# Optimization experiments

Measured on AMD Instinct MI355X. Metric: run time of the kernel, lower is better.

## Reference

```python
import jax, jax.numpy as jnp
import numpy as np
import math

B, T, C, H = 4, 2048, 1024, 16
D = C // H
NEG = -1.0e9

def setup_inputs() -> dict:
    key = jax.random.key(0)
    k_x, k_wa, k_wp = jax.random.split(key, 3)
    x = jax.random.normal(k_x, (B, T, C), dtype=jnp.float32)
    # causal additive-mask input, shape [B, T, T] as the forward branch expects
    mask = jnp.broadcast_to(jnp.tril(jnp.ones((T, T), dtype=jnp.float32)), (B, T, T))
    W_attn = jax.random.normal(k_wa, (C, 3 * C), dtype=jnp.float32) * (1.0 / math.sqrt(C))
    b_attn = jnp.zeros((3 * C,), dtype=jnp.float32)
    W_proj = jax.random.normal(k_wp, (C, C), dtype=jnp.float32) * (1.0 / math.sqrt(C))
    b_proj = jnp.zeros((C,), dtype=jnp.float32)
    return {"x": x, "mask": mask, "W_attn": W_attn, "b_attn": b_attn,
            "W_proj": W_proj, "b_proj": b_proj}

def reference(x, mask, W_attn, b_attn, W_proj, b_proj):
    # fused QKV projection: [B,T,3C]
    qkv = x @ W_attn + b_attn
    q, k, v = jnp.split(qkv, 3, axis=-1)
    q = q.reshape(B, T, H, D)
    k = k.reshape(B, T, H, D)
    v = v.reshape(B, T, H, D)
    # scores [B,H,T,T]
    att = jnp.einsum('bqhd,bkhd->bhqk', q, k) * (1.0 / math.sqrt(D))
    # additive custom mask: att += -1e9 * (1 - mask), broadcast over heads
    att = att + NEG * (1.0 - mask)[:, None, :, :]
    att = jax.nn.softmax(att, axis=-1)  # dropout p=0 -> identity
    y = jnp.einsum('bhqk,bkhd->bqhd', att, v).reshape(B, T, C)
    return y @ W_proj + b_proj
```

## Files before the change

kernel.cpp:

```cpp
#include <hip/hip_runtime.h>
#include <hip/hip_bf16.h>

#define Bq 4
#define Tq 2048
#define Cq 1024
#define Hq 16
#define Dq 64
#define Mq (Bq*Tq)
#define N3q (3*Cq)

typedef __attribute__((ext_vector_type(8))) short   short8;
typedef __attribute__((ext_vector_type(4))) float   f32x4;
typedef __attribute__((ext_vector_type(4))) unsigned int u32x4;
typedef __attribute__((ext_vector_type(4))) unsigned short ushort4v;
typedef unsigned short u16;
typedef unsigned int u32;

__device__ __forceinline__ void gld_lds16(const u16* g, u16* l) {
  __builtin_amdgcn_global_load_lds(
      (const __attribute__((address_space(1))) unsigned int*)g,
      (__attribute__((address_space(3))) unsigned int*)l, 16, 0, 0);
}

__device__ __forceinline__ u16 f2bf(float f) {
  return __builtin_bit_cast(u16, __float2bfloat16(f));
}
__device__ __forceinline__ u16 f2bf_fast(float f) {
  u32 u = __builtin_bit_cast(u32, f);
  return (u16)((u + 0x8000u) >> 16);
}
__device__ __forceinline__ float fexp2(float x) {
  return __builtin_amdgcn_exp2f(x);
}

__device__ __forceinline__ f32x4 mfma16(short8 a, short8 b, f32x4 c) {
  return __builtin_amdgcn_mfma_f32_16x16x32_bf16(a, b, c, 0, 0, 0);
}

__global__ void cvt_bf16(const float* __restrict__ in, u16* __restrict__ out, int n) {
  int i = (blockIdx.x * 256 + threadIdx.x) * 4;
  if (i < n) {
    float4 v = *(const float4*)(in + i);
    ushort4v o;
    o.x = f2bf_fast(v.x); o.y = f2bf_fast(v.y);
    o.z = f2bf_fast(v.z); o.w = f2bf_fast(v.w);
    *(ushort4v*)(out + i) = o;
  }
}

__global__ void transpose_cvt(const float* __restrict__ in, u16* __restrict__ out,
                              int R, int C) {
  __shared__ float tile[32][33];
  int j0 = blockIdx.x * 32;
  int i0 = blockIdx.y * 32;
  int c = threadIdx.x & 31, r0 = threadIdx.x >> 5;
#pragma unroll
  for (int rr = 0; rr < 32; rr += 8)
    tile[r0 + rr][c] = in[(size_t)(i0 + r0 + rr) * C + j0 + c];
  __syncthreads();
#pragma unroll
  for (int rr = 0; rr < 32; rr += 8) {
    int j = r0 + rr;
    out[(size_t)(j0 + j) * R + i0 + c] = f2bf_fast(tile[c][j]);
  }
}

template<int OUT_MODE>
__global__ __launch_bounds__(256, 2) void gemm_bt(
    const u16* __restrict__ A, const u16* __restrict__ Bt,
    const float* __restrict__ bias, void* __restrict__ Dp,
    int M, int N, int K)
{
  __shared__ __align__(16) u16 lA[2][128 * 64];
  __shared__ __align__(16) u16 lB[2][128 * 64];
  const int t = threadIdx.x;
  const int l = t & 63, w = t >> 6;
  const int bn = blockIdx.x, bm = blockIdx.y;
  const int wr = (w >> 1) * 64, wc = (w & 1) * 64;

  const int srow = t >> 3;
  const int scol = 8 * ((t & 7) ^ (srow & 7));
  const u16* ga = A  + (size_t)(bm * 128 + srow) * K + scol;
  const u16* gb = Bt + (size_t)(bn * 128 + srow) * K + scol;

  f32x4 acc[4][4] = {};

#define STAGE_BT(buf, k0_) {                                              \
    _Pragma("unroll")                                                     \
    for (int c = 0; c < 4; ++c) {                                         \
      gld_lds16(ga + (size_t)(32 * c) * K + (k0_), &lA[buf][c * 2048 + w * 512]); \
      gld_lds16(gb + (size_t)(32 * c) * K + (k0_), &lB[buf][c * 2048 + w * 512]); \
    } }

  STAGE_BT(0, 0);
  asm volatile("s_waitcnt vmcnt(0)" ::: "memory");
  __syncthreads();

  int c2 = 0;
  for (int k0 = 0; k0 < K; k0 += 64) {
    const bool more = (k0 + 64 < K);
    if (more) STAGE_BT(c2 ^ 1, k0 + 64);

    short8 af[4][2], bf[4][2];
#pragma unroll
    for (int m = 0; m < 4; ++m)
#pragma unroll
      for (int kk = 0; kk < 2; ++kk) {
        int ar = wr + m * 16 + (l & 15);
        int slot = (kk * 4 + (l >> 4)) ^ (l & 7);
        af[m][kk] = *(const short8*)&lA[c2][ar * 64 + slot * 8];
        int br = wc + m * 16 + (l & 15);
        bf[m][kk] = *(const short8*)&lB[c2][br * 64 + slot * 8];
      }
    __builtin_amdgcn_s_setprio(1);
#pragma unroll
    for (int kk = 0; kk < 2; ++kk)
#pragma unroll
      for (int m = 0; m < 4; ++m)
#pragma unroll
        for (int n = 0; n < 4; ++n)
          acc[m][n] = mfma16(af[m][kk], bf[n][kk], acc[m][n]);
    __builtin_amdgcn_s_setprio(0);

    if (more) {
      asm volatile("s_waitcnt vmcnt(0)" ::: "memory");
      __syncthreads();
      c2 ^= 1;
    }
  }
#undef STAGE_BT

  float bv[4];
#pragma unroll
  for (int n = 0; n < 4; ++n) bv[n] = bias[bn * 128 + wc + n * 16 + (l & 15)];

  if (OUT_MODE == 2) {
    const int col0 = bn * 128 + wc;
    const int p  = col0 >> 10;
    const int hh = (col0 >> 6) & 15;
    u16* qb = (u16*)Dp;
#pragma unroll
    for (int m = 0; m < 4; ++m)
#pragma unroll
      for (int r = 0; r < 4; ++r) {
        int row = bm * 128 + wr + m * 16 + (l >> 4) * 4 + r;
        int bb = row >> 11, tt = row & 2047;
        u16* dst = qb + (((size_t)(p * 64 + bb * 16 + hh) * 2048 + tt) * 64) + (l & 15);
#pragma unroll
        for (int n = 0; n < 4; ++n)
          dst[n * 16] = f2bf_fast(acc[m][n][r] + bv[n]);
      }
  } else {
#pragma unroll
    for (int m = 0; m < 4; ++m)
#pragma unroll
      for (int r = 0; r < 4; ++r) {
        int row = bm * 128 + wr + m * 16 + (l >> 4) * 4 + r;
        size_t base = (size_t)row * N + bn * 128 + wc + (l & 15);
#pragma unroll
        for (int n = 0; n < 4; ++n)
          ((float*)Dp)[base + n * 16] = acc[m][n][r] + bv[n];
      }
  }
}

__global__ __launch_bounds__(1024, 4) void flash_attn(
    const u16* __restrict__ qkvh, u16* __restrict__ Y)
{
  __shared__ __align__(16) u16 Kl[2][64 * 64];
  __shared__ __align__(16) u16 Vt[2][64 * 64];

  const int t = threadIdx.x, l = t & 63, w = t >> 6;
  const int wg  = w & 3;
  const int g   = l >> 4;
  const int id   = blockIdx.x + 4 * blockIdx.y;
  const int xcd  = id & 7;
  const int rest = id >> 3;
  const int x    = rest & 3;
  const int gg   = rest >> 2;
  const int bh   = xcd + 8 * gg;
  const int b = bh >> 4, h = bh & 15;
  const int grp = w >> 2;
  const int qA = 4 * x + grp, qB = 31 - qA;
  const int jmaxb = 31 - 4 * x;

  const size_t hbase = (size_t)(b * Hq + h) * (size_t)(Tq * Dq);
  const u16* Qh = qkvh + hbase;
  const u16* Kh = qkvh + (size_t)64  * (Tq * Dq) + hbase;
  const u16* Vh = qkvh + (size_t)128 * (Tq * Dq) + hbase;

  short8 qfA[2], qfB[2];
  {
    const u16* qp = Qh + (size_t)(qA * 64 + wg * 16 + (l & 15)) * 64;
    qfA[0] = *(const short8*)(qp + (g * 8));
    qfA[1] = *(const short8*)(qp + 32 + (g * 8));
    const u16* qp2 = Qh + (size_t)(qB * 64 + wg * 16 + (l & 15)) * 64;
    qfB[0] = *(const short8*)(qp2 + (g * 8));
    qfB[1] = *(const short8*)(qp2 + 32 + (g * 8));
  }

  float mA = -1e30f, lsA = 0.f, mB = -1e30f, lsB = 0.f;
  f32x4 oA[4] = {}, oB[4] = {};

  const int ksrow = t >> 3;
  const int kscol = 8 * ((t & 7) ^ (ksrow & 7));
  const int vkey = t & 63;
  const int vdj  = w - 8;

  const int srcA = ((g << 1) & 3) * 16 + (l & 15);
  const int srcB = (((g << 1) + 1) & 3) * 16 + (l & 15);
  const bool sel = (g >> 1) != 0;

  if (w < 8) {
    gld_lds16(Kh + (size_t)ksrow * 64 + kscol, &Kl[0][w * 512]);
  } else {
    short8 vr = *(const short8*)(Vh + (size_t)vkey * 64 + vdj * 8);
    asm volatile("s_waitcnt vmcnt(0)" ::: "memory");
#pragma unroll
    for (int i = 0; i < 8; ++i)
      Vt[0][(vdj * 8 + i) * 64 + (((vkey >> 3) ^ i) * 8) + (vkey & 7)] = (u16)vr[i];
  }
  __syncthreads();

  int cur = 0;
  for (int j = 0; j <= jmaxb; ++j) {
    short8 vrn;
    if (j < jmaxb) {
      const size_t krow1 = (size_t)(j + 1) * 64;
      if (w < 8)
        gld_lds16(Kh + (krow1 + ksrow) * 64 + kscol, &Kl[cur ^ 1][w * 512]);
      else
        vrn = *(const short8*)(Vh + (krow1 + vkey) * 64 + vdj * 8);
    }

#pragma unroll
    for (int strip = 0; strip < 2; ++strip) {
      const int qb = strip ? qB : qA;
      if (j > qb) continue;
      const short8* qf = strip ? qfB : qfA;
      float& m  = strip ? mB : mA;
      float& ls = strip ? lsB : lsA;
      f32x4* oacc = strip ? oB : oA;

      f32x4 s4[4] = {};
#pragma unroll
      for (int kk = 0; kk < 2; ++kk)
#pragma unroll
        for (int n = 0; n < 4; ++n) {
          int key = n * 16 + (l & 15);
          int slot = (kk * 4 + g) ^ (key & 7);
          short8 kf = *(const short8*)&Kl[cur][key * 64 + slot * 8];
          s4[n] = mfma16(kf, qf[kk], s4[n]);
        }

      if (j == qb) {
        const int q = wg * 16 + (l & 15);
#pragma unroll
        for (int n = 0; n < 4; ++n)
#pragma unroll
          for (int r = 0; r < 4; ++r)
            if (n * 16 + g * 4 + r > q) s4[n][r] = -1e30f;
      }

      const float SC = 0.18033688011112042f;
      float mx01 = fmaxf(fmaxf(s4[0][0], s4[0][1]), fmaxf(s4[0][2], s4[0][3]));
      float mx1  = fmaxf(fmaxf(s4[1][0], s4[1][1]), fmaxf(s4[1][2], s4[1][3]));
      float mx2  = fmaxf(fmaxf(s4[2][0], s4[2][1]), fmaxf(s4[2][2], s4[2][3]));
      float mx3  = fmaxf(fmaxf(s4[3][0], s4[3][1]), fmaxf(s4[3][2], s4[3][3]));
      float mx = fmaxf(fmaxf(mx01, mx1), fmaxf(mx2, mx3));
      mx = fmaxf(mx, __shfl_xor(mx, 16));
      mx = fmaxf(mx, __shfl_xor(mx, 32));
      if (!__all(mx - m <= 8.f)) {
        float mn = fmaxf(m, mx);
        float fac = fexp2((m - mn) * SC);
        ls *= fac;
#pragma unroll
        for (int dn = 0; dn < 4; ++dn)
#pragma unroll
          for (int r = 0; r < 4; ++r) oacc[dn][r] *= fac;
        m = mn;
      }
      const float nm = -m * SC;
      float rs = 0.f;
#pragma unroll
      for (int n = 0; n < 4; ++n)
#pragma unroll
        for (int r = 0; r < 4; ++r) {
          float p = fexp2(fmaf(s4[n][r], SC, nm));
          s4[n][r] = p;
          rs += p;
        }
      rs += __shfl_xor(rs, 16);
      rs += __shfl_xor(rs, 32);
      ls += rs;

      u32 pk[4][2];
#pragma unroll
      for (int n = 0; n < 4; ++n) {
        pk[n][0] = (u32)f2bf(s4[n][0]) | ((u32)f2bf(s4[n][1]) << 16);
        pk[n][1] = (u32)f2bf(s4[n][2]) | ((u32)f2bf(s4[n][3]) << 16);
      }

      short8 pf[2];
#pragma unroll
      for (int kk = 0; kk < 2; ++kk) {
        u32 t00 = (u32)__shfl((int)pk[2 * kk][0], srcA);
        u32 t10 = (u32)__shfl((int)pk[2 * kk + 1][0], srcA);
        u32 t01 = (u32)__shfl((int)pk[2 * kk][1], srcA);
        u32 t11 = (u32)__shfl((int)pk[2 * kk + 1][1], srcA);
        u32 u00 = (u32)__shfl((int)pk[2 * kk][0], srcB);
        u32 u10 = (u32)__shfl((int)pk[2 * kk + 1][0], srcB);
        u32 u01 = (u32)__shfl((int)pk[2 * kk][1], srcB);
        u32 u11 = (u32)__shfl((int)pk[2 * kk + 1][1], srcB);
        u32x4 fr;
        fr.x = sel ? t10 : t00;
        fr.y = sel ? t11 : t01;
        fr.z = sel ? u10 : u00;
        fr.w = sel ? u11 : u01;
        pf[kk] = __builtin_bit_cast(short8, fr);
      }

#pragma unroll
      for (int kk = 0; kk < 2; ++kk) {
        int slot = (kk * 4 + g) ^ (l & 7);
        short8 pfk = pf[kk];
#pragma unroll
        for (int dn = 0; dn < 4; ++dn) {
          int d = dn * 16 + (l & 15);
          short8 vf = *(const short8*)&Vt[cur][d * 64 + slot * 8];
          oacc[dn] = mfma16(vf, pfk, oacc[dn]);
        }
      }
    }

    if (j < jmaxb && w >= 8) {
      asm volatile("s_waitcnt vmcnt(0)" ::: "memory");
#pragma unroll
      for (int i = 0; i < 8; ++i)
        Vt[cur ^ 1][(vdj * 8 + i) * 64 + (((vkey >> 3) ^ i) * 8) + (vkey & 7)] = (u16)vrn[i];
    }
    __syncthreads();
    cur ^= 1;
  }

#pragma unroll
  for (int strip = 0; strip < 2; ++strip) {
    const int qb = strip ? qB : qA;
    float ls = strip ? lsB : lsA;
    f32x4* oacc = strip ? oB : oA;
    float inv = 1.f / ls;
    size_t row = (size_t)(b * Tq + qb * 64 + wg * 16 + (l & 15));
    u16* yp = Y + row * Cq + h * 64 + g * 4;
#pragma unroll
    for (int dn = 0; dn < 4; ++dn) {
      ushort4v ov;
      ov.x = f2bf(oacc[dn][0] * inv);
      ov.y = f2bf(oacc[dn][1] * inv);
      ov.z = f2bf(oacc[dn][2] * inv);
      ov.w = f2bf(oacc[dn][3] * inv);
      *(ushort4v*)(yp + dn * 16) = ov;
    }
  }
}

extern "C" void kernel_launch(void* const* d_in, const int* in_sizes, int n_in,
                              void* d_out, int out_size, void* d_ws, size_t ws_size,
                              hipStream_t stream)
{
  const float* x      = (const float*)d_in[0];
  const float* W_attn = (const float*)d_in[2];
  const float* b_attn = (const float*)d_in[3];
  const float* W_proj = (const float*)d_in[4];
  const float* b_proj = (const float*)d_in[5];

  char* ws = (char*)d_ws;
  u16* x_bf    = (u16*)ws; ws += (size_t)Mq * Cq * 2;
  u16* wqkv_t  = (u16*)ws; ws += (size_t)N3q * Cq * 2;
  u16* wproj_t = (u16*)ws; ws += (size_t)Cq * Cq * 2;
  u16* qkvh    = (u16*)ws; ws += (size_t)Mq * N3q * 2;
  u16* y       = (u16*)ws; ws += (size_t)Mq * Cq * 2;
  if ((size_t)(ws - (char*)d_ws) > ws_size) return;

  cvt_bf16<<<(Mq * Cq / 4 + 255) / 256, 256, 0, stream>>>(x, x_bf, Mq * Cq);
  transpose_cvt<<<dim3(N3q / 32, Cq / 32), 256, 0, stream>>>(W_attn, wqkv_t, Cq, N3q);
  transpose_cvt<<<dim3(Cq / 32, Cq / 32), 256, 0, stream>>>(W_proj, wproj_t, Cq, Cq);

  gemm_bt<2><<<dim3(N3q / 128, Mq / 128), 256, 0, stream>>>(
      x_bf, wqkv_t, b_attn, (void*)qkvh, Mq, N3q, Cq);

  flash_attn<<<dim3(4, Bq * Hq), 1024, 0, stream>>>(qkvh, y);

  gemm_bt<0><<<dim3(Cq / 128, Mq / 128), 256, 0, stream>>>(
      y, wproj_t, b_proj, d_out, Mq, Cq, Cq);
}
```

Measured before the change: 187.6 us.

## Halve flash-attention block size and double grid with balanced causal scheduling

Result: no change. 187.8 us (+0.1%).

```diff
diff --git a/kernel.cpp b/kernel.cpp
--- a/kernel.cpp
+++ b/kernel.cpp
@@ -164,7 +164,7 @@
   }
 }
 
-__global__ __launch_bounds__(1024, 4) void flash_attn(
+__global__ __launch_bounds__(512, 4) void flash_attn(
     const u16* __restrict__ qkvh, u16* __restrict__ Y)
 {
   __shared__ __align__(16) u16 Kl[2][64 * 64];
@@ -173,16 +173,18 @@
   const int t = threadIdx.x, l = t & 63, w = t >> 6;
   const int wg  = w & 3;
   const int g   = l >> 4;
-  const int id   = blockIdx.x + 4 * blockIdx.y;
-  const int xcd  = id & 7;
-  const int rest = id >> 3;
-  const int x    = rest & 3;
-  const int gg   = rest >> 2;
-  const int bh   = xcd + 8 * gg;
+  const int id  = blockIdx.x + 8 * blockIdx.y;
+  const int hi  = id >> 8;
+  const int lo  = id & 255;
+  const int xcd = lo & 7;
+  const int u   = lo >> 3;
+  const int bh  = xcd + 8 * (u & 7);
+  const int xpair = u >> 3;
+  const int x   = hi ? (7 - xpair) : xpair;
   const int b = bh >> 4, h = bh & 15;
   const int grp = w >> 2;
-  const int qA = 4 * x + grp, qB = 31 - qA;
-  const int jmaxb = 31 - 4 * x;
+  const int qA = 2 * x + grp, qB = 31 - qA;
+  const int jmaxb = 31 - 2 * x;
 
   const size_t hbase = (size_t)(b * Hq + h) * (size_t)(Tq * Dq);
   const u16* Qh = qkvh + hbase;
@@ -202,35 +204,59 @@
   float mA = -1e30f, lsA = 0.f, mB = -1e30f, lsB = 0.f;
   f32x4 oA[4] = {}, oB[4] = {};
 
-  const int ksrow = t >> 3;
-  const int kscol = 8 * ((t & 7) ^ (ksrow & 7));
-  const int vkey = t & 63;
-  const int vdj  = w - 8;
-
   const int srcA = ((g << 1) & 3) * 16 + (l & 15);
   const int srcB = (((g << 1) + 1) & 3) * 16 + (l & 15);
   const bool sel = (g >> 1) != 0;
 
-  if (w < 8) {
-    gld_lds16(Kh + (size_t)ksrow * 64 + kscol, &Kl[0][w * 512]);
+  if (w < 4) {
+#pragma unroll
+    for (int c = 0; c < 2; ++c) {
+      int i = t + 256 * c;
+      int row = i >> 3;
+      int col = 8 * ((i & 7) ^ (row & 7));
+      gld_lds16(Kh + (size_t)row * 64 + col, &Kl[0][c * 2048 + w * 512]);
+    }
   } else {
-    short8 vr = *(const short8*)(Vh + (size_t)vkey * 64 + vdj * 8);
+    short8 vr[2];
+#pragma unroll
+    for (int c = 0; c < 2; ++c) {
+      int i = (t - 256) + 256 * c;
+      int key = i & 63, dj = i >> 6;
+      vr[c] = *(const short8*)(Vh + (size_t)key * 64 + dj * 8);
+    }
     asm volatile("s_waitcnt vmcnt(0)" ::: "memory");
 #pragma unroll
-    for (int i = 0; i < 8; ++i)
-      Vt[0][(vdj * 8 + i) * 64 + (((vkey >> 3) ^ i) * 8) + (vkey & 7)] = (u16)vr[i];
+    for (int c = 0; c < 2; ++c) {
+      int i = (t - 256) + 256 * c;
+      int key = i & 63, dj = i >> 6;
+#pragma unroll
+      for (int ii = 0; ii < 8; ++ii)
+        Vt[0][(dj * 8 + ii) * 64 + (((key >> 3) ^ ii) * 8) + (key & 7)] = (u16)vr[c][ii];
+    }
   }
   __syncthreads();
 
   int cur = 0;
   for (int j = 0; j <= jmaxb; ++j) {
-    short8 vrn;
+    short8 vrn[2];
     if (j < jmaxb) {
       const size_t krow1 = (size_t)(j + 1) * 64;
-      if (w < 8)
-        gld_lds16(Kh + (krow1 + ksrow) * 64 + kscol, &Kl[cur ^ 1][w * 512]);
-      else
-        vrn = *(const short8*)(Vh + (krow1 + vkey) * 64 + vdj * 8);
+      if (w < 4) {
+#pragma unroll
+        for (int c = 0; c < 2; ++c) {
+          int i = t + 256 * c;
+          int row = i >> 3;
+          int col = 8 * ((i & 7) ^ (row & 7));
+          gld_lds16(Kh + (krow1 + row) * 64 + col, &Kl[cur ^ 1][c * 2048 + w * 512]);
+        }
+      } else {
+#pragma unroll
+        for (int c = 0; c < 2; ++c) {
+          int i = (t - 256) + 256 * c;
+          int key = i & 63, dj = i >> 6;
+          vrn[c] = *(const short8*)(Vh + (krow1 + key) * 64 + dj * 8);
+        }
+      }
     }
 
 #pragma unroll
@@ -333,11 +359,16 @@
       }
     }
 
-    if (j < jmaxb && w >= 8) {
+    if (j < jmaxb && w >= 4) {
       asm volatile("s_waitcnt vmcnt(0)" ::: "memory");
 #pragma unroll
-      for (int i = 0; i < 8; ++i)
-        Vt[cur ^ 1][(vdj * 8 + i) * 64 + (((vkey >> 3) ^ i) * 8) + (vkey & 7)] = (u16)vrn[i];
+      for (int c = 0; c < 2; ++c) {
+        int i = (t - 256) + 256 * c;
+        int key = i & 63, dj = i >> 6;
+#pragma unroll
+        for (int ii = 0; ii < 8; ++ii)
+          Vt[cur ^ 1][(dj * 8 + ii) * 64 + (((key >> 3) ^ ii) * 8) + (key & 7)] = (u16)vrn[c][ii];
+      }
     }
     __syncthreads();
     cur ^= 1;
@@ -388,7 +419,7 @@
   gemm_bt<2><<<dim3(N3q / 128, Mq / 128), 256, 0, stream>>>(
       x_bf, wqkv_t, b_attn, (void*)qkvh, Mq, N3q, Cq);
 
-  flash_attn<<<dim3(4, Bq * Hq), 1024, 0, stream>>>(qkvh, y);
+  flash_attn<<<dim3(8, Bq * Hq), 512, 0, stream>>>(qkvh, y);
 
   gemm_bt<0><<<dim3(Cq / 128, Mq / 128), 256, 0, stream>>>(
       y, wproj_t, b_proj, d_out, Mq, Cq, Cq);
```
